# Kernel tuning notes

Measured on AMD Instinct MI355X. Metric: run time of the kernel, lower is better.

The kernel has to match this reference:

```python
import jax, jax.numpy as jnp
import numpy as np

N = 50000          # nodes
E = 800000         # directed edges (before self-loops)
NUM_CLASSES = 10
NEG_SLOPE = 0.2    # PyG GATConv default leaky_relu slope


def segment_softmax(logits, seg, num_segments):
    # numerically stable softmax over edges grouped by target node
    m = jax.ops.segment_max(logits, seg, num_segments=num_segments)
    e = jnp.exp(logits - m[seg])
    s = jax.ops.segment_sum(e, seg, num_segments=num_segments)
    return e / s[seg]


def gat_conv(x, src, dst, W, a_src, a_dst, b, n_nodes):
    # single-head PyG-style GATConv (eval mode: attention dropout disabled)
    h = x @ W                              # [N, C]
    alpha_src = h @ a_src                  # [N]
    alpha_dst = h @ a_dst                  # [N]
    logits = jax.nn.leaky_relu(alpha_src[src] + alpha_dst[dst], NEG_SLOPE)  # [E']
    alpha = segment_softmax(logits, dst, n_nodes)                            # [E']
    out = jax.ops.segment_sum(h[src] * alpha[:, None], dst, num_segments=n_nodes)
    return out + b


def setup_inputs() -> dict:
    key = jax.random.key(0)
    ks = jax.random.split(key, 13)
    x = jax.random.normal(ks[0], (N, 11), dtype=jnp.float32)
    edge_index = jax.random.randint(ks[1], (2, E), 0, N, dtype=jnp.int32)
    batch = jnp.zeros((N,), dtype=jnp.int32)  # unused by forward (no pooling)
    s = 0.1
    W1 = jax.random.normal(ks[2], (11, 16), jnp.float32) * s
    a1_src = jax.random.normal(ks[3], (16,), jnp.float32) * s
    a1_dst = jax.random.normal(ks[4], (16,), jnp.float32) * s
    b1 = jnp.zeros((16,), jnp.float32)
    W2 = jax.random.normal(ks[5], (16, 64), jnp.float32) * s
    a2_src = jax.random.normal(ks[6], (64,), jnp.float32) * s
    a2_dst = jax.random.normal(ks[7], (64,), jnp.float32) * s
    b2 = jnp.zeros((64,), jnp.float32)
    Wl = jax.random.normal(ks[8], (64, NUM_CLASSES), jnp.float32) * s
    bl = jnp.zeros((NUM_CLASSES,), jnp.float32)
    return {"x": x, "edge_index": edge_index, "batch": batch,
            "W1": W1, "a1_src": a1_src, "a1_dst": a1_dst, "b1": b1,
            "W2": W2, "a2_src": a2_src, "a2_dst": a2_dst, "b2": b2,
            "Wl": Wl, "bl": bl}


def reference(x, edge_index, batch, W1, a1_src, a1_dst, b1,
              W2, a2_src, a2_dst, b2, Wl, bl):
    n = x.shape[0]
    loop = jnp.arange(n, dtype=edge_index.dtype)
    src = jnp.concatenate([edge_index[0], loop])  # add self-loops (PyG default)
    dst = jnp.concatenate([edge_index[1], loop])
    h = gat_conv(x, src, dst, W1, a1_src, a1_dst, b1, n)
    h = jax.nn.relu(h)
    h = gat_conv(h, src, dst, W2, a2_src, a2_dst, b2, n)
    return h @ Wl + bl
```

## Files before the change

kernel.cpp:

```cpp
#include <hip/hip_runtime.h>
#include <hip/hip_bf16.h>

#define NEG_SLOPE 0.2f
#define BUCK 128
#define BSTRIDE 4096

__device__ __forceinline__ float lrelu(float x) {
    return x > 0.f ? x : NEG_SLOPE * x;
}

__global__ __launch_bounds__(256)
void front_kernel(const float* __restrict__ x,
                  const float* __restrict__ W1,
                  const float* __restrict__ a1s, const float* __restrict__ a1d,
                  float* __restrict__ h, float* __restrict__ as, float* __restrict__ ad,
                  int n, int tb,
                  const float* __restrict__ W2,
                  const float* __restrict__ a2s, const float* __restrict__ a2d,
                  const float* __restrict__ b2,
                  const float* __restrict__ Wl, const float* __restrict__ bl,
                  float* __restrict__ va, float* __restrict__ vd,
                  float* __restrict__ Wc, float* __restrict__ bc,
                  int* __restrict__ gcur, int nbuck) {
    const int bid = blockIdx.x;
    if (bid < tb) {
        constexpr int F_IN = 11, C_OUT = 16;
        __shared__ float sW[F_IN * C_OUT];
        __shared__ float sAs[C_OUT];
        __shared__ float sAd[C_OUT];
        for (int i = threadIdx.x; i < F_IN * C_OUT; i += 256) sW[i] = W1[i];
        if (threadIdx.x < C_OUT) { sAs[threadIdx.x] = a1s[threadIdx.x]; sAd[threadIdx.x] = a1d[threadIdx.x]; }
        __syncthreads();
        int i = bid * 256 + threadIdx.x;
        if (i >= n) return;
        float xin[F_IN];
#pragma unroll
        for (int f = 0; f < F_IN; ++f) xin[f] = x[(size_t)i * F_IN + f];
        float s_acc = 0.f, d_acc = 0.f;
#pragma unroll
        for (int c = 0; c < C_OUT; ++c) {
            float acc = 0.f;
#pragma unroll
            for (int f = 0; f < F_IN; ++f) acc = fmaf(xin[f], sW[f * C_OUT + c], acc);
            h[(size_t)i * C_OUT + c] = acc;
            s_acc = fmaf(acc, sAs[c], s_acc);
            d_acc = fmaf(acc, sAd[c], d_acc);
        }
        as[i] = s_acc;
        ad[i] = d_acc;
    } else {
        int t = threadIdx.x;
        for (int i = t; i < nbuck; i += 256) gcur[i] = i * BSTRIDE;
        if (t < 16) {
            float s = 0.f, s2 = 0.f;
            for (int c = 0; c < 64; ++c) {
                float w = W2[t * 64 + c];
                s = fmaf(w, a2s[c], s);
                s2 = fmaf(w, a2d[c], s2);
            }
            va[t] = s; vd[t] = s2;
        }
        int i = t - 64;
        if (i >= 0 && i < 160) {
            int f = i / 10, k = i % 10;
            float s = 0.f;
            for (int c = 0; c < 64; ++c) s = fmaf(W2[f * 64 + c], Wl[c * 10 + k], s);
            Wc[i] = s;
        }
        int k2 = t - 240;
        if (k2 >= 0 && k2 < 10) {
            float s = bl[k2];
            for (int c = 0; c < 64; ++c) s = fmaf(b2[c], Wl[c * 10 + k2], s);
            bc[k2] = s;
        }
    }
}

__global__ __launch_bounds__(256)
void scatter_kernel(const int* __restrict__ ei, int E, int n, int CH,
                    int* __restrict__ gcur, unsigned int* __restrict__ pk, int nbuck) {
    __shared__ int lhist[512];
    for (int i = threadIdx.x; i < nbuck; i += 256) lhist[i] = 0;
    __syncthreads();
    const int beg = blockIdx.x * CH;
    const int end = min(beg + CH, E + n);
    for (int e = beg + threadIdx.x * 4; e < end; e += 1024) {
        if (e + 3 < E) {
            const int4 d4 = *reinterpret_cast<const int4*>(&ei[E + e]);
            atomicAdd(&lhist[d4.x >> 7], 1);
            atomicAdd(&lhist[d4.y >> 7], 1);
            atomicAdd(&lhist[d4.z >> 7], 1);
            atomicAdd(&lhist[d4.w >> 7], 1);
        } else {
            for (int k = 0; k < 4 && e + k < end; ++k) {
                int ee = e + k;
                int d = (ee < E) ? ei[E + ee] : (ee - E);
                atomicAdd(&lhist[d >> 7], 1);
            }
        }
    }
    __syncthreads();
    for (int i = threadIdx.x; i < nbuck; i += 256) {
        int c = lhist[i];
        lhist[i] = (c > 0) ? atomicAdd(&gcur[i], c) : 0;
    }
    __syncthreads();
    for (int e = beg + threadIdx.x * 4; e < end; e += 1024) {
        if (e + 3 < E) {
            const int4 s4 = *reinterpret_cast<const int4*>(&ei[e]);
            const int4 d4 = *reinterpret_cast<const int4*>(&ei[E + e]);
            int slot;
            slot = atomicAdd(&lhist[d4.x >> 7], 1);
            pk[slot] = ((unsigned int)(d4.x & 127) << 25) | (unsigned int)s4.x;
            slot = atomicAdd(&lhist[d4.y >> 7], 1);
            pk[slot] = ((unsigned int)(d4.y & 127) << 25) | (unsigned int)s4.y;
            slot = atomicAdd(&lhist[d4.z >> 7], 1);
            pk[slot] = ((unsigned int)(d4.z & 127) << 25) | (unsigned int)s4.z;
            slot = atomicAdd(&lhist[d4.w >> 7], 1);
            pk[slot] = ((unsigned int)(d4.w & 127) << 25) | (unsigned int)s4.w;
        } else {
            for (int k = 0; k < 4 && e + k < end; ++k) {
                int ee = e + k;
                int s, d;
                if (ee < E) { s = ei[ee]; d = ei[E + ee]; } else { s = d = ee - E; }
                int slot = atomicAdd(&lhist[d >> 7], 1);
                pk[slot] = ((unsigned int)(d & 127) << 25) | (unsigned int)s;
            }
        }
    }
}

__global__ __launch_bounds__(256)
void bucketsort_kernel(const unsigned int* __restrict__ pk,
                       const int* __restrict__ gcur,
                       int* __restrict__ csrc,
                       int* __restrict__ row_beg, int* __restrict__ deg,
                       int n) {
    __shared__ int lcnt[BUCK];
    __shared__ int lofs[BUCK];
    const int tid = threadIdx.x;
    const int base = blockIdx.x * BUCK;
    const int beg = blockIdx.x * BSTRIDE;
    const int end = gcur[blockIdx.x];

    if (tid < BUCK) lcnt[tid] = 0;
    __syncthreads();
    for (int i = beg + tid * 4; i < end; i += 1024) {
        if (i + 3 < end) {
            const uint4 p4 = *reinterpret_cast<const uint4*>(&pk[i]);
            atomicAdd(&lcnt[p4.x >> 25], 1);
            atomicAdd(&lcnt[p4.y >> 25], 1);
            atomicAdd(&lcnt[p4.z >> 25], 1);
            atomicAdd(&lcnt[p4.w >> 25], 1);
        } else {
            for (int k = 0; k < 4 && i + k < end; ++k)
                atomicAdd(&lcnt[pk[i + k] >> 25], 1);
        }
    }
    __syncthreads();
    int v = 0;
    if (tid < BUCK) { v = lcnt[tid]; lofs[tid] = v; }
    __syncthreads();
    for (int off = 1; off < BUCK; off <<= 1) {
        int u = 0;
        if (tid < BUCK && tid >= off) u = lofs[tid - off];
        __syncthreads();
        if (tid < BUCK && tid >= off) lofs[tid] += u;
        __syncthreads();
    }
    if (tid < BUCK) {
        int excl = lofs[tid] - v;
        if (base + tid < n) {
            row_beg[base + tid] = beg + excl;
            deg[base + tid] = v;
        }
        lcnt[tid] = excl;
    }
    __syncthreads();
    for (int i = beg + tid * 4; i < end; i += 1024) {
        if (i + 3 < end) {
            const uint4 p4 = *reinterpret_cast<const uint4*>(&pk[i]);
            int slot;
            slot = beg + atomicAdd(&lcnt[p4.x >> 25], 1); csrc[slot] = (int)(p4.x & 0x1FFFFFFu);
            slot = beg + atomicAdd(&lcnt[p4.y >> 25], 1); csrc[slot] = (int)(p4.y & 0x1FFFFFFu);
            slot = beg + atomicAdd(&lcnt[p4.z >> 25], 1); csrc[slot] = (int)(p4.z & 0x1FFFFFFu);
            slot = beg + atomicAdd(&lcnt[p4.w >> 25], 1); csrc[slot] = (int)(p4.w & 0x1FFFFFFu);
        } else {
            for (int k = 0; k < 4 && i + k < end; ++k) {
                unsigned int p = pk[i + k];
                int slot = beg + atomicAdd(&lcnt[p >> 25], 1);
                csrc[slot] = (int)(p & 0x1FFFFFFu);
            }
        }
    }
}

__global__ void gat_agg1_kernel(const int* __restrict__ row_beg,
                                const int* __restrict__ deg,
                                const int* __restrict__ csrc,
                                const float* __restrict__ as,
                                const float* __restrict__ ad,
                                const float* __restrict__ h,
                                const float* __restrict__ b1,
                                const float* __restrict__ va,
                                const float* __restrict__ vd,
                                float* __restrict__ X1r,
                                float* __restrict__ as2,
                                float* __restrict__ ad2, int n) {
    constexpr int C = 16;
    __shared__ float sb1[16], sva[16], svd[16];
    if (threadIdx.x < 16) {
        sb1[threadIdx.x] = b1[threadIdx.x];
        sva[threadIdx.x] = va[threadIdx.x];
        svd[threadIdx.x] = vd[threadIdx.x];
    }
    __syncthreads();
    int node = (blockIdx.x * blockDim.x + threadIdx.x) >> 4;
    int sl = threadIdx.x & 15;
    if (node >= n) return;
    int beg = row_beg[node];
    int end = beg + deg[node];
    float add = ad[node];

    const int eq = sl >> 2;
    const int cl = sl & 3;
    float lsum = 0.f;
    float4 acc = {0.f, 0.f, 0.f, 0.f};
    for (int chunk = beg; chunk < end; chunk += 16) {
        int e = chunk + sl;
        float wv = 0.f; int sv = 0;
        if (e < end) {
            sv = csrc[e];
            wv = __expf(lrelu(as[sv] + add));
            lsum += wv;
        }
        const int nch = min(16, end - chunk);
        const int T = (nch + 3) >> 2;
        for (int t = 0; t < T; ++t) {
            int j = t * 4 + eq;
            float wj = __shfl(wv, j, 16);
            int   sj = __shfl(sv, j, 16);
            if (j < nch) {
                const float4 hv = *reinterpret_cast<const float4*>(&h[(size_t)sj * C + cl * 4]);
                acc.x = fmaf(wj, hv.x, acc.x);
                acc.y = fmaf(wj, hv.y, acc.y);
                acc.z = fmaf(wj, hv.z, acc.z);
                acc.w = fmaf(wj, hv.w, acc.w);
            }
        }
    }
#pragma unroll
    for (int k = 1; k < 16; k <<= 1) lsum += __shfl_xor(lsum, k, 16);
#pragma unroll
    for (int k = 4; k < 16; k <<= 1) {
        acc.x += __shfl_xor(acc.x, k, 16);
        acc.y += __shfl_xor(acc.y, k, 16);
        acc.z += __shfl_xor(acc.z, k, 16);
        acc.w += __shfl_xor(acc.w, k, 16);
    }
    float inv = 1.f / lsum;
    float x0 = fmaxf(fmaf(acc.x, inv, sb1[cl * 4 + 0]), 0.f);
    float x1 = fmaxf(fmaf(acc.y, inv, sb1[cl * 4 + 1]), 0.f);
    float x2 = fmaxf(fmaf(acc.z, inv, sb1[cl * 4 + 2]), 0.f);
    float x3 = fmaxf(fmaf(acc.w, inv, sb1[cl * 4 + 3]), 0.f);
    if (eq == 0) {
        float4 o = {x0, x1, x2, x3};
        *reinterpret_cast<float4*>(&X1r[(size_t)node * C + cl * 4]) = o;
    }
    float p = x0 * sva[cl * 4] + x1 * sva[cl * 4 + 1] + x2 * sva[cl * 4 + 2] + x3 * sva[cl * 4 + 3];
    float q = x0 * svd[cl * 4] + x1 * svd[cl * 4 + 1] + x2 * svd[cl * 4 + 2] + x3 * svd[cl * 4 + 3];
    p += __shfl_xor(p, 1, 16); p += __shfl_xor(p, 2, 16);
    q += __shfl_xor(q, 1, 16); q += __shfl_xor(q, 2, 16);
    if (sl == 0) { as2[node] = p; ad2[node] = q; }
}

__global__ void gat_agg2_kernel(const int* __restrict__ row_beg,
                                const int* __restrict__ deg,
                                const int* __restrict__ csrc,
                                const float* __restrict__ as2,
                                const float* __restrict__ ad2,
                                const float* __restrict__ X1r,
                                const float* __restrict__ Wc,
                                const float* __restrict__ bc,
                                float* __restrict__ out, int n) {
    constexpr int C = 16;
    __shared__ float sWc[160], sbc[10];
    for (int i = threadIdx.x; i < 160; i += blockDim.x) sWc[i] = Wc[i];
    if (threadIdx.x < 10) sbc[threadIdx.x] = bc[threadIdx.x];
    __syncthreads();
    int node = (blockIdx.x * blockDim.x + threadIdx.x) >> 4;
    int sl = threadIdx.x & 15;
    if (node >= n) return;
    int beg = row_beg[node];
    int end = beg + deg[node];
    float add = ad2[node];

    const int eq = sl >> 2;
    const int cl = sl & 3;
    float lsum = 0.f;
    float4 acc = {0.f, 0.f, 0.f, 0.f};
    for (int chunk = beg; chunk < end; chunk += 16) {
        int e = chunk + sl;
        float wv = 0.f; int sv = 0;
        if (e < end) {
            sv = csrc[e];
            wv = __expf(lrelu(as2[sv] + add));
            lsum += wv;
        }
        const int nch = min(16, end - chunk);
        const int T = (nch + 3) >> 2;
        for (int t = 0; t < T; ++t) {
            int j = t * 4 + eq;
            float wj = __shfl(wv, j, 16);
            int   sj = __shfl(sv, j, 16);
            if (j < nch) {
                const float4 hv = *reinterpret_cast<const float4*>(&X1r[(size_t)sj * C + cl * 4]);
                acc.x = fmaf(wj, hv.x, acc.x);
                acc.y = fmaf(wj, hv.y, acc.y);
                acc.z = fmaf(wj, hv.z, acc.z);
                acc.w = fmaf(wj, hv.w, acc.w);
            }
        }
    }
#pragma unroll
    for (int k = 1; k < 16; k <<= 1) lsum += __shfl_xor(lsum, k, 16);
#pragma unroll
    for (int k = 4; k < 16; k <<= 1) {
        acc.x += __shfl_xor(acc.x, k, 16);
        acc.y += __shfl_xor(acc.y, k, 16);
        acc.z += __shfl_xor(acc.z, k, 16);
        acc.w += __shfl_xor(acc.w, k, 16);
    }
    float inv = 1.f / lsum;
    acc.x *= inv; acc.y *= inv; acc.z *= inv; acc.w *= inv;
    float p[10];
#pragma unroll
    for (int k = 0; k < 10; ++k) {
        p[k] = acc.x * sWc[(cl * 4 + 0) * 10 + k]
             + acc.y * sWc[(cl * 4 + 1) * 10 + k]
             + acc.z * sWc[(cl * 4 + 2) * 10 + k]
             + acc.w * sWc[(cl * 4 + 3) * 10 + k];
    }
#pragma unroll
    for (int k = 0; k < 10; ++k) {
        p[k] += __shfl_xor(p[k], 1, 16);
        p[k] += __shfl_xor(p[k], 2, 16);
    }
    if (sl < 10) {
        float v = p[0];
#pragma unroll
        for (int k = 1; k < 10; ++k) v = (sl == k) ? p[k] : v;
        out[(size_t)node * 10 + sl] = v + sbc[sl];
    }
}

extern "C" void kernel_launch(void* const* d_in, const int* in_sizes, int n_in,
                              void* d_out, int out_size, void* d_ws, size_t ws_size,
                              hipStream_t stream) {
    const float* x       = (const float*)d_in[0];
    const int*   ei      = (const int*)d_in[1];
    const float* W1      = (const float*)d_in[3];
    const float* a1_src  = (const float*)d_in[4];
    const float* a1_dst  = (const float*)d_in[5];
    const float* b1      = (const float*)d_in[6];
    const float* W2      = (const float*)d_in[7];
    const float* a2_src  = (const float*)d_in[8];
    const float* a2_dst  = (const float*)d_in[9];
    const float* b2      = (const float*)d_in[10];
    const float* Wl      = (const float*)d_in[11];
    const float* bl      = (const float*)d_in[12];
    float* out = (float*)d_out;

    const int N = in_sizes[2];
    const int E = in_sizes[1] / 2;
    const int ET = E + N;

    const int B = 256;
    auto cdiv = [](int a, int b) { return (a + b - 1) / b; };

    const int NBUCK = cdiv(N, BUCK);
    const int NBLK  = 512;
    const int CHB   = ((cdiv(ET, NBLK) + 3) / 4) * 4;
    const int TB    = cdiv(N, B);

    char* ws = (char*)d_ws;
    size_t off = 0;
    auto alloc = [&](size_t bytes) {
        char* p = ws + off;
        off = (off + bytes + 255) & ~(size_t)255;
        return p;
    };
    float*        h1   = (float*)alloc((size_t)N * 16 * 4);
    float*        X1r  = (float*)alloc((size_t)N * 16 * 4);
    float*        as1  = (float*)alloc((size_t)N * 4);
    float*        ad1  = (float*)alloc((size_t)N * 4);
    float*        as2  = (float*)alloc((size_t)N * 4);
    float*        ad2  = (float*)alloc((size_t)N * 4);
    int*          rowb = (int*)alloc((size_t)N * 4);
    int*          degb = (int*)alloc((size_t)N * 4);
    int*          csrc = (int*)alloc((size_t)NBUCK * BSTRIDE * 4);
    unsigned int* pk   = (unsigned int*)alloc((size_t)NBUCK * BSTRIDE * 4);
    int*          gcur = (int*)alloc((size_t)NBUCK * 4);
    float*        va   = (float*)alloc(16 * 4);
    float*        vd   = (float*)alloc(16 * 4);
    float*        Wc   = (float*)alloc(160 * 4);
    float*        bc   = (float*)alloc(10 * 4);
    (void)ws_size;

    front_kernel<<<TB + 1, B, 0, stream>>>(
        x, W1, a1_src, a1_dst, h1, as1, ad1, N, TB,
        W2, a2_src, a2_dst, b2, Wl, bl, va, vd, Wc, bc, gcur, NBUCK);

    scatter_kernel<<<NBLK, B, 0, stream>>>(ei, E, N, CHB, gcur, pk, NBUCK);

    bucketsort_kernel<<<NBUCK, 256, 0, stream>>>(pk, gcur, csrc, rowb, degb, N);

    gat_agg1_kernel<<<cdiv(N * 16, B), B, 0, stream>>>(rowb, degb, csrc, as1, ad1, h1, b1, va, vd, X1r, as2, ad2, N);

    gat_agg2_kernel<<<cdiv(N * 16, B), B, 0, stream>>>(rowb, degb, csrc, as2, ad2, X1r, Wc, bc, out, N);
}
```

Measured before the change: 69.83 us.

## Store node features in fp16 and precompute layer-1 edge weights during scatter

Node feature buffers h1 and X1r are now stored as fp16, which halves the bytes of the random gathers in both aggregation kernels. Layer-1 attention weights exp(lrelu(as+ad)) are computed in the scatter kernel and carried through the bucket sort as an 8-byte (src, weight) record, so agg1 no longer gathers as1 per edge. The trade-off is double the bytes moved through scatter and bucketsort, extra random reads of as1/ad1 in scatter, and reduced feature precision.

```diff
diff --git a/kernel.cpp b/kernel.cpp
--- a/kernel.cpp
+++ b/kernel.cpp
@@ -1,9 +1,11 @@
 #include <hip/hip_runtime.h>
 #include <hip/hip_bf16.h>
+#include <hip/hip_fp16.h>
 
 #define NEG_SLOPE 0.2f
 #define BUCK 128
 #define BSTRIDE 4096
+#define SRCM 0x1FFFFFFu
 
 __device__ __forceinline__ float lrelu(float x) {
     return x > 0.f ? x : NEG_SLOPE * x;
@@ -13,7 +15,7 @@
 void front_kernel(const float* __restrict__ x,
                   const float* __restrict__ W1,
                   const float* __restrict__ a1s, const float* __restrict__ a1d,
-                  float* __restrict__ h, float* __restrict__ as, float* __restrict__ ad,
+                  __half* __restrict__ h, float* __restrict__ as, float* __restrict__ ad,
                   int n, int tb,
                   const float* __restrict__ W2,
                   const float* __restrict__ a2s, const float* __restrict__ a2d,
@@ -36,16 +38,26 @@
         float xin[F_IN];
 #pragma unroll
         for (int f = 0; f < F_IN; ++f) xin[f] = x[(size_t)i * F_IN + f];
+        float r[C_OUT];
         float s_acc = 0.f, d_acc = 0.f;
 #pragma unroll
         for (int c = 0; c < C_OUT; ++c) {
             float acc = 0.f;
 #pragma unroll
             for (int f = 0; f < F_IN; ++f) acc = fmaf(xin[f], sW[f * C_OUT + c], acc);
-            h[(size_t)i * C_OUT + c] = acc;
+            r[c] = acc;
             s_acc = fmaf(acc, sAs[c], s_acc);
             d_acc = fmaf(acc, sAd[c], d_acc);
         }
+        unsigned int u[8];
+#pragma unroll
+        for (int k = 0; k < 8; ++k) {
+            __half2 hh = __floats2half2_rn(r[2 * k], r[2 * k + 1]);
+            u[k] = *reinterpret_cast<unsigned int*>(&hh);
+        }
+        uint4* hp = reinterpret_cast<uint4*>(&h[(size_t)i * 16]);
+        hp[0] = make_uint4(u[0], u[1], u[2], u[3]);
+        hp[1] = make_uint4(u[4], u[5], u[6], u[7]);
         as[i] = s_acc;
         ad[i] = d_acc;
     } else {
@@ -78,7 +90,8 @@
 
 __global__ __launch_bounds__(256)
 void scatter_kernel(const int* __restrict__ ei, int E, int n, int CH,
-                    int* __restrict__ gcur, unsigned int* __restrict__ pk, int nbuck) {
+                    int* __restrict__ gcur, uint2* __restrict__ pk, int nbuck,
+                    const float* __restrict__ as1, const float* __restrict__ ad1) {
     __shared__ int lhist[512];
     for (int i = threadIdx.x; i < nbuck; i += 256) lhist[i] = 0;
     __syncthreads();
@@ -109,31 +122,36 @@
         if (e + 3 < E) {
             const int4 s4 = *reinterpret_cast<const int4*>(&ei[e]);
             const int4 d4 = *reinterpret_cast<const int4*>(&ei[E + e]);
+            float w0 = __expf(lrelu(as1[s4.x] + ad1[d4.x]));
+            float w1 = __expf(lrelu(as1[s4.y] + ad1[d4.y]));
+            float w2 = __expf(lrelu(as1[s4.z] + ad1[d4.z]));
+            float w3 = __expf(lrelu(as1[s4.w] + ad1[d4.w]));
             int slot;
             slot = atomicAdd(&lhist[d4.x >> 7], 1);
-            pk[slot] = ((unsigned int)(d4.x & 127) << 25) | (unsigned int)s4.x;
+            pk[slot] = make_uint2(((unsigned int)(d4.x & 127) << 25) | (unsigned int)s4.x, __float_as_uint(w0));
             slot = atomicAdd(&lhist[d4.y >> 7], 1);
-            pk[slot] = ((unsigned int)(d4.y & 127) << 25) | (unsigned int)s4.y;
+            pk[slot] = make_uint2(((unsigned int)(d4.y & 127) << 25) | (unsigned int)s4.y, __float_as_uint(w1));
             slot = atomicAdd(&lhist[d4.z >> 7], 1);
-            pk[slot] = ((unsigned int)(d4.z & 127) << 25) | (unsigned int)s4.z;
+            pk[slot] = make_uint2(((unsigned int)(d4.z & 127) << 25) | (unsigned int)s4.z, __float_as_uint(w2));
             slot = atomicAdd(&lhist[d4.w >> 7], 1);
-            pk[slot] = ((unsigned int)(d4.w & 127) << 25) | (unsigned int)s4.w;
+            pk[slot] = make_uint2(((unsigned int)(d4.w & 127) << 25) | (unsigned int)s4.w, __float_as_uint(w3));
         } else {
             for (int k = 0; k < 4 && e + k < end; ++k) {
                 int ee = e + k;
                 int s, d;
                 if (ee < E) { s = ei[ee]; d = ei[E + ee]; } else { s = d = ee - E; }
+                float w = __expf(lrelu(as1[s] + ad1[d]));
                 int slot = atomicAdd(&lhist[d >> 7], 1);
-                pk[slot] = ((unsigned int)(d & 127) << 25) | (unsigned int)s;
+                pk[slot] = make_uint2(((unsigned int)(d & 127) << 25) | (unsigned int)s, __float_as_uint(w));
             }
         }
     }
 }
 
 __global__ __launch_bounds__(256)
-void bucketsort_kernel(const unsigned int* __restrict__ pk,
+void bucketsort_kernel(const uint2* __restrict__ pk,
                        const int* __restrict__ gcur,
-                       int* __restrict__ csrc,
+                       uint2* __restrict__ cw,
                        int* __restrict__ row_beg, int* __restrict__ deg,
                        int n) {
     __shared__ int lcnt[BUCK];
@@ -145,16 +163,13 @@
 
     if (tid < BUCK) lcnt[tid] = 0;
     __syncthreads();
-    for (int i = beg + tid * 4; i < end; i += 1024) {
-        if (i + 3 < end) {
-            const uint4 p4 = *reinterpret_cast<const uint4*>(&pk[i]);
-            atomicAdd(&lcnt[p4.x >> 25], 1);
-            atomicAdd(&lcnt[p4.y >> 25], 1);
-            atomicAdd(&lcnt[p4.z >> 25], 1);
-            atomicAdd(&lcnt[p4.w >> 25], 1);
+    for (int i = beg + tid * 2; i < end; i += 512) {
+        if (i + 1 < end) {
+            const uint4 q = *reinterpret_cast<const uint4*>(&pk[i]);
+            atomicAdd(&lcnt[q.x >> 25], 1);
+            atomicAdd(&lcnt[q.z >> 25], 1);
         } else {
-            for (int k = 0; k < 4 && i + k < end; ++k)
-                atomicAdd(&lcnt[pk[i + k] >> 25], 1);
+            atomicAdd(&lcnt[pk[i].x >> 25], 1);
         }
     }
     __syncthreads();
@@ -177,37 +192,30 @@
         lcnt[tid] = excl;
     }
     __syncthreads();
-    for (int i = beg + tid * 4; i < end; i += 1024) {
-        if (i + 3 < end) {
-            const uint4 p4 = *reinterpret_cast<const uint4*>(&pk[i]);
+    for (int i = beg + tid * 2; i < end; i += 512) {
+        if (i + 1 < end) {
+            const uint4 q = *reinterpret_cast<const uint4*>(&pk[i]);
             int slot;
-            slot = beg + atomicAdd(&lcnt[p4.x >> 25], 1); csrc[slot] = (int)(p4.x & 0x1FFFFFFu);
-            slot = beg + atomicAdd(&lcnt[p4.y >> 25], 1); csrc[slot] = (int)(p4.y & 0x1FFFFFFu);
-            slot = beg + atomicAdd(&lcnt[p4.z >> 25], 1); csrc[slot] = (int)(p4.z & 0x1FFFFFFu);
-            slot = beg + atomicAdd(&lcnt[p4.w >> 25], 1); csrc[slot] = (int)(p4.w & 0x1FFFFFFu);
+            slot = beg + atomicAdd(&lcnt[q.x >> 25], 1); cw[slot] = make_uint2(q.x, q.y);
+            slot = beg + atomicAdd(&lcnt[q.z >> 25], 1); cw[slot] = make_uint2(q.z, q.w);
         } else {
-            for (int k = 0; k < 4 && i + k < end; ++k) {
-                unsigned int p = pk[i + k];
-                int slot = beg + atomicAdd(&lcnt[p >> 25], 1);
-                csrc[slot] = (int)(p & 0x1FFFFFFu);
-            }
+            const uint2 q = pk[i];
+            int slot = beg + atomicAdd(&lcnt[q.x >> 25], 1);
+            cw[slot] = q;
         }
     }
 }
 
 __global__ void gat_agg1_kernel(const int* __restrict__ row_beg,
                                 const int* __restrict__ deg,
-                                const int* __restrict__ csrc,
-                                const float* __restrict__ as,
-                                const float* __restrict__ ad,
-                                const float* __restrict__ h,
+                                const uint2* __restrict__ cw,
+                                const __half* __restrict__ h,
                                 const float* __restrict__ b1,
                                 const float* __restrict__ va,
                                 const float* __restrict__ vd,
-                                float* __restrict__ X1r,
+                                __half* __restrict__ X1r,
                                 float* __restrict__ as2,
                                 float* __restrict__ ad2, int n) {
-    constexpr int C = 16;
     __shared__ float sb1[16], sva[16], svd[16];
     if (threadIdx.x < 16) {
         sb1[threadIdx.x] = b1[threadIdx.x];
@@ -220,7 +228,6 @@
     if (node >= n) return;
     int beg = row_beg[node];
     int end = beg + deg[node];
-    float add = ad[node];
 
     const int eq = sl >> 2;
     const int cl = sl & 3;
@@ -230,8 +237,9 @@
         int e = chunk + sl;
         float wv = 0.f; int sv = 0;
         if (e < end) {
-            sv = csrc[e];
-            wv = __expf(lrelu(as[sv] + add));
+            uint2 rec = cw[e];
+            sv = (int)(rec.x & SRCM);
+            wv = __uint_as_float(rec.y);
             lsum += wv;
         }
         const int nch = min(16, end - chunk);
@@ -241,11 +249,13 @@
             float wj = __shfl(wv, j, 16);
             int   sj = __shfl(sv, j, 16);
             if (j < nch) {
-                const float4 hv = *reinterpret_cast<const float4*>(&h[(size_t)sj * C + cl * 4]);
-                acc.x = fmaf(wj, hv.x, acc.x);
-                acc.y = fmaf(wj, hv.y, acc.y);
-                acc.z = fmaf(wj, hv.z, acc.z);
-                acc.w = fmaf(wj, hv.w, acc.w);
+                uint2 hv2 = *reinterpret_cast<const uint2*>(&h[(size_t)sj * 16 + cl * 4]);
+                float2 f01 = __half22float2(*reinterpret_cast<__half2*>(&hv2.x));
+                float2 f23 = __half22float2(*reinterpret_cast<__half2*>(&hv2.y));
+                acc.x = fmaf(wj, f01.x, acc.x);
+                acc.y = fmaf(wj, f01.y, acc.y);
+                acc.z = fmaf(wj, f23.x, acc.z);
+                acc.w = fmaf(wj, f23.y, acc.w);
             }
         }
     }
@@ -264,8 +274,11 @@
     float x2 = fmaxf(fmaf(acc.z, inv, sb1[cl * 4 + 2]), 0.f);
     float x3 = fmaxf(fmaf(acc.w, inv, sb1[cl * 4 + 3]), 0.f);
     if (eq == 0) {
-        float4 o = {x0, x1, x2, x3};
-        *reinterpret_cast<float4*>(&X1r[(size_t)node * C + cl * 4]) = o;
+        __half2 p01 = __floats2half2_rn(x0, x1);
+        __half2 p23 = __floats2half2_rn(x2, x3);
+        uint2 o = make_uint2(*reinterpret_cast<unsigned int*>(&p01),
+                             *reinterpret_cast<unsigned int*>(&p23));
+        *reinterpret_cast<uint2*>(&X1r[(size_t)node * 16 + cl * 4]) = o;
     }
     float p = x0 * sva[cl * 4] + x1 * sva[cl * 4 + 1] + x2 * sva[cl * 4 + 2] + x3 * sva[cl * 4 + 3];
     float q = x0 * svd[cl * 4] + x1 * svd[cl * 4 + 1] + x2 * svd[cl * 4 + 2] + x3 * svd[cl * 4 + 3];
@@ -276,14 +289,13 @@
 
 __global__ void gat_agg2_kernel(const int* __restrict__ row_beg,
                                 const int* __restrict__ deg,
-                                const int* __restrict__ csrc,
+                                const uint2* __restrict__ cw,
                                 const float* __restrict__ as2,
                                 const float* __restrict__ ad2,
-                                const float* __restrict__ X1r,
+                                const __half* __restrict__ X1r,
                                 const float* __restrict__ Wc,
                                 const float* __restrict__ bc,
                                 float* __restrict__ out, int n) {
-    constexpr int C = 16;
     __shared__ float sWc[160], sbc[10];
     for (int i = threadIdx.x; i < 160; i += blockDim.x) sWc[i] = Wc[i];
     if (threadIdx.x < 10) sbc[threadIdx.x] = bc[threadIdx.x];
@@ -303,7 +315,7 @@
         int e = chunk + sl;
         float wv = 0.f; int sv = 0;
         if (e < end) {
-            sv = csrc[e];
+            sv = (int)(cw[e].x & SRCM);
             wv = __expf(lrelu(as2[sv] + add));
             lsum += wv;
         }
@@ -314,11 +326,13 @@
             float wj = __shfl(wv, j, 16);
             int   sj = __shfl(sv, j, 16);
             if (j < nch) {
-                const float4 hv = *reinterpret_cast<const float4*>(&X1r[(size_t)sj * C + cl * 4]);
-                acc.x = fmaf(wj, hv.x, acc.x);
-                acc.y = fmaf(wj, hv.y, acc.y);
-                acc.z = fmaf(wj, hv.z, acc.z);
-                acc.w = fmaf(wj, hv.w, acc.w);
+                uint2 hv2 = *reinterpret_cast<const uint2*>(&X1r[(size_t)sj * 16 + cl * 4]);
+                float2 f01 = __half22float2(*reinterpret_cast<__half2*>(&hv2.x));
+                float2 f23 = __half22float2(*reinterpret_cast<__half2*>(&hv2.y));
+                acc.x = fmaf(wj, f01.x, acc.x);
+                acc.y = fmaf(wj, f01.y, acc.y);
+                acc.z = fmaf(wj, f23.x, acc.z);
+                acc.w = fmaf(wj, f23.y, acc.w);
             }
         }
     }
@@ -390,16 +404,16 @@
         off = (off + bytes + 255) & ~(size_t)255;
         return p;
     };
-    float*        h1   = (float*)alloc((size_t)N * 16 * 4);
-    float*        X1r  = (float*)alloc((size_t)N * 16 * 4);
+    __half*       h1   = (__half*)alloc((size_t)N * 16 * 2);
+    __half*       X1r  = (__half*)alloc((size_t)N * 16 * 2);
     float*        as1  = (float*)alloc((size_t)N * 4);
     float*        ad1  = (float*)alloc((size_t)N * 4);
     float*        as2  = (float*)alloc((size_t)N * 4);
     float*        ad2  = (float*)alloc((size_t)N * 4);
     int*          rowb = (int*)alloc((size_t)N * 4);
     int*          degb = (int*)alloc((size_t)N * 4);
-    int*          csrc = (int*)alloc((size_t)NBUCK * BSTRIDE * 4);
-    unsigned int* pk   = (unsigned int*)alloc((size_t)NBUCK * BSTRIDE * 4);
+    uint2*        cw   = (uint2*)alloc((size_t)NBUCK * BSTRIDE * 8);
+    uint2*        pk   = (uint2*)alloc((size_t)NBUCK * BSTRIDE * 8);
     int*          gcur = (int*)alloc((size_t)NBUCK * 4);
     float*        va   = (float*)alloc(16 * 4);
     float*        vd   = (float*)alloc(16 * 4);
@@ -411,11 +425,11 @@
         x, W1, a1_src, a1_dst, h1, as1, ad1, N, TB,
         W2, a2_src, a2_dst, b2, Wl, bl, va, vd, Wc, bc, gcur, NBUCK);
 
-    scatter_kernel<<<NBLK, B, 0, stream>>>(ei, E, N, CHB, gcur, pk, NBUCK);
-
-    bucketsort_kernel<<<NBUCK, 256, 0, stream>>>(pk, gcur, csrc, rowb, degb, N);
-
-    gat_agg1_kernel<<<cdiv(N * 16, B), B, 0, stream>>>(rowb, degb, csrc, as1, ad1, h1, b1, va, vd, X1r, as2, ad2, N);
-
-    gat_agg2_kernel<<<cdiv(N * 16, B), B, 0, stream>>>(rowb, degb, csrc, as2, ad2, X1r, Wc, bc, out, N);
-}
+    scatter_kernel<<<NBLK, B, 0, stream>>>(ei, E, N, CHB, gcur, pk, NBUCK, as1, ad1);
+
+    bucketsort_kernel<<<NBUCK, 256, 0, stream>>>(pk, gcur, cw, rowb, degb, N);
+
+    gat_agg1_kernel<<<cdiv(N * 16, B), B, 0, stream>>>(rowb, degb, cw, h1, b1, va, vd, X1r, as2, ad2, N);
+
+    gat_agg2_kernel<<<cdiv(N * 16, B), B, 0, stream>>>(rowb, degb, cw, as2, ad2, X1r, Wc, bc, out, N);
+}
```

Measured after the change: 70.78 us. Within noise of the previous version (+1.4%).
